# Kernel optimization log

Hardware: AMD Instinct MI355X
Metric: run time of the kernel (lower is better)

Reference implementation:

```python
import jax, jax.numpy as jnp
import numpy as np
from math import sqrt, pi

EMBED, HEADS, ATTN, MLP = 1024, 16, 1024, 4096
HEAD_DIM = ATTN // HEADS
EPS = 1e-5

def _ln(x):
    mu = jnp.mean(x, axis=-1, keepdims=True)
    var = jnp.var(x, axis=-1, keepdims=True)
    return (x - mu) / jnp.sqrt(var + EPS)

def _gelu(x):
    return 0.5 * x * (1.0 + jnp.tanh(sqrt(2.0 / pi) * (x + 0.044715 * x**3)))

def setup_inputs() -> dict:
    key = jax.random.key(0)
    ks = jax.random.split(key, 6)
    B, S = 2, 2048
    x = jax.random.normal(ks[0], (B, S, EMBED), dtype=jnp.float32)
    # weights stored as [in, out] (transpose of torch's [out, in]); math identical
    w_qkv = jax.random.normal(ks[1], (EMBED, 3 * ATTN), dtype=jnp.float32) / sqrt(EMBED)
    w_fc = jax.random.normal(ks[2], (ATTN, EMBED), dtype=jnp.float32) / sqrt(ATTN)
    w1 = jax.random.normal(ks[3], (EMBED, MLP), dtype=jnp.float32) / sqrt(EMBED)
    b1 = jnp.zeros((MLP,), dtype=jnp.float32)
    w2 = jax.random.normal(ks[4], (MLP, EMBED), dtype=jnp.float32) / sqrt(MLP)
    b2 = jnp.zeros((EMBED,), dtype=jnp.float32)
    return {"x": x, "w_qkv": w_qkv, "w_fc": w_fc, "w1": w1, "b1": b1, "w2": w2, "b2": b2}

def reference(x, w_qkv, w_fc, w1, b1, w2, b2):
    B, S, _ = x.shape
    res = x
    h = _ln(x)
    qkv = h @ w_qkv                                   # [B,S,3*ATTN]
    q, k, v = jnp.split(qkv, 3, axis=-1)
    q = q.reshape(B, S, HEADS, HEAD_DIM)
    k = k.reshape(B, S, HEADS, HEAD_DIM)
    v = v.reshape(B, S, HEADS, HEAD_DIM)
    attn = jnp.einsum('bqnc,bknc->bnqk', q, k) / sqrt(HEAD_DIM)  # [B,H,S,S]
    attn = jax.nn.softmax(attn, axis=-1)
    attn_val = jnp.einsum('bnqk,bknc->bqnc', attn, v).reshape(B, S, ATTN)
    x = res + attn_val @ w_fc
    res = x
    h = _ln(x)
    h = _gelu(h @ w1 + b1) @ w2 + b2
    return res + h
```

## Files before the change

kernel.cpp:

```cpp
#include <hip/hip_runtime.h>

typedef unsigned short u16;
typedef __attribute__((ext_vector_type(8))) short bf16x8;
typedef __attribute__((ext_vector_type(4))) short s16x4;
typedef __attribute__((ext_vector_type(4))) float f32x4;

#define DEV __device__ __forceinline__

DEV u16 f2bf(float f) {
  union { float f; unsigned u; } v; v.f = f;
  unsigned r = v.u + 0x7fffu + ((v.u >> 16) & 1u);
  return (u16)(r >> 16);
}
DEV u16 f2bf_tr(float f) {
  union { float f; unsigned u; } v; v.f = f;
  return (u16)(v.u >> 16);
}

DEV int swzi(int row, int col) { return row * 64 + (col ^ ((row & 7) << 3)); }

DEV void gl16(const u16* g, u16* l) {
  __builtin_amdgcn_global_load_lds((const __attribute__((address_space(1))) void*)g,
                                   (__attribute__((address_space(3))) void*)l, 16, 0, 0);
}

template <int N> DEV void waitv() {
  asm volatile("s_waitcnt vmcnt(%0)" :: "n"(N) : "memory");
}

__global__ __launch_bounds__(256) void wcastT(const float* __restrict__ w,
                                              u16* __restrict__ wt, int K, int N) {
  __shared__ float t[32][33];
  int n0 = blockIdx.x * 32, k0 = blockIdx.y * 32;
  int tx = threadIdx.x & 31, ty = threadIdx.x >> 5;
#pragma unroll
  for (int i = 0; i < 32; i += 8)
    t[ty + i][tx] = w[(size_t)(k0 + ty + i) * N + n0 + tx];
  __syncthreads();
#pragma unroll
  for (int i = 0; i < 32; i += 8)
    wt[(size_t)(n0 + ty + i) * K + k0 + tx] = f2bf(t[tx][ty + i]);
}

__global__ __launch_bounds__(256) void ln_kernel(const float* __restrict__ x,
                                                 u16* __restrict__ out) {
  int row = blockIdx.x, tid = threadIdx.x;
  const float4* xr = (const float4*)(x + (size_t)row * 1024);
  float4 f = xr[tid];
  float s = f.x + f.y + f.z + f.w;
  float s2 = f.x * f.x + f.y * f.y + f.z * f.z + f.w * f.w;
#pragma unroll
  for (int o = 1; o < 64; o <<= 1) { s += __shfl_xor(s, o); s2 += __shfl_xor(s2, o); }
  __shared__ float red[2][4];
  int wid = tid >> 6;
  if ((tid & 63) == 0) { red[0][wid] = s; red[1][wid] = s2; }
  __syncthreads();
  float tot  = red[0][0] + red[0][1] + red[0][2] + red[0][3];
  float tot2 = red[1][0] + red[1][1] + red[1][2] + red[1][3];
  float mu = tot * (1.0f / 1024.0f);
  float var = tot2 * (1.0f / 1024.0f) - mu * mu;
  float rstd = rsqrtf(var + 1e-5f);
  s16x4 o4;
  o4[0] = (short)f2bf((f.x - mu) * rstd);
  o4[1] = (short)f2bf((f.y - mu) * rstd);
  o4[2] = (short)f2bf((f.z - mu) * rstd);
  o4[3] = (short)f2bf((f.w - mu) * rstd);
  *(s16x4*)(out + (size_t)row * 1024 + tid * 4) = o4;
}

template <int MODE, int BM, int BK>
__global__ __launch_bounds__(256) void gemm_bt(
    const u16* __restrict__ A, const u16* __restrict__ Bt, int N, int K,
    const float* __restrict__ resid, const float* __restrict__ bias,
    float* __restrict__ outF, u16* __restrict__ o0, u16* __restrict__ o1,
    u16* __restrict__ o2) {
  constexpr int MR = BM / 32;
  constexpr int KH = BK / 32;
  constexpr int LDEPTH = KH * (BM / 64 + 2);
  constexpr int ACH = BM * 32, BCH = 128 * 32;
  __shared__ __align__(16) u16 lA[2 * KH * ACH];
  __shared__ __align__(16) u16 lB[2 * KH * BCH];
  int tid = threadIdx.x;
  int lane = tid & 63, wid = tid >> 6;
  int lr = lane & 15, lg = lane >> 4;

  int gx = gridDim.x;
  int nwg = gx * gridDim.y;
  int bid = blockIdx.y * gx + blockIdx.x;
  int swz = (bid & 7) * (nwg >> 3) + (bid >> 3);
  int rowBase = (swz / gx) * BM, colBase = (swz % gx) * 128;
  int wr = (wid >> 1) * (MR * 16), wc = (wid & 1) * 64;

  int srow = wid * 16 + (lane >> 2);
  int scol = (lane & 3) * 8;
  const u16* gA = A + (size_t)(rowBase + srow) * K + scol;
  const u16* gB = Bt + (size_t)(colBase + srow) * K + scol;
  u16* lAb = &lA[wid * 16 * 32];
  u16* lBb = &lB[wid * 16 * 32];

  auto stage = [&](int t, int buf) {
    int k0 = t * BK;
#pragma unroll
    for (int kk = 0; kk < KH; kk++) {
      u16* dA = lAb + buf * KH * ACH + kk * ACH;
      u16* dB = lBb + buf * KH * BCH + kk * BCH;
      int koff = k0 + kk * 32;
#pragma unroll
      for (int c = 0; c < BM / 64; c++)
        gl16(gA + (size_t)c * 64 * K + koff, dA + c * 64 * 32);
#pragma unroll
      for (int c = 0; c < 2; c++)
        gl16(gB + (size_t)c * 64 * K + koff, dB + c * 64 * 32);
    }
  };

  f32x4 acc[MR][4];
  f32x4 zero = {0.f, 0.f, 0.f, 0.f};
#pragma unroll
  for (int m = 0; m < MR; m++)
#pragma unroll
    for (int n = 0; n < 4; n++) acc[m][n] = zero;

  stage(0, 0);

  int nt = K / BK;
  for (int t = 0; t < nt; t++) {
    int cur = t & 1;
    if (t + 1 < nt) {
      stage(t + 1, cur ^ 1);
      waitv<LDEPTH>();
    } else {
      waitv<0>();
    }
    __builtin_amdgcn_s_barrier();
    asm volatile("" ::: "memory");

    const u16* cA = &lA[cur * KH * ACH];
    const u16* cB = &lB[cur * KH * BCH];
#pragma unroll
    for (int kk = 0; kk < KH; kk++) {
      bf16x8 af[MR], bfv[4];
#pragma unroll
      for (int m = 0; m < MR; m++)
        af[m] = *(const bf16x8*)&cA[kk * ACH + (wr + m * 16 + lr) * 32 + lg * 8];
#pragma unroll
      for (int n = 0; n < 4; n++)
        bfv[n] = *(const bf16x8*)&cB[kk * BCH + (wc + n * 16 + lr) * 32 + lg * 8];
#pragma unroll
      for (int m = 0; m < MR; m++)
#pragma unroll
        for (int n = 0; n < 4; n++)
          acc[m][n] = __builtin_amdgcn_mfma_f32_16x16x32_bf16(bfv[n], af[m], acc[m][n], 0, 0, 0);
    }

    asm volatile("" ::: "memory");
    __builtin_amdgcn_s_barrier();
  }

#pragma unroll
  for (int m = 0; m < MR; m++) {
    int grow = rowBase + wr + m * 16 + lr;
#pragma unroll
    for (int n = 0; n < 4; n++) {
      int gcol = colBase + wc + n * 16 + lg * 4;
      f32x4 v4 = acc[m][n];
      if constexpr (MODE == 0) {
        if (gcol < 2048) {
          bool isq = gcol < 1024;
          u16* dst = isq ? o0 : o1;
          s16x4 o4;
#pragma unroll
          for (int j = 0; j < 4; j++)
            o4[j] = (short)f2bf(isq ? v4[j] * 0.18033688011112042f : v4[j]);
          *(s16x4*)&dst[(size_t)grow * 1024 + (gcol & 1023)] = o4;
        } else {
          int c = gcol - 2048;
          int bb = grow >> 11, ss = grow & 2047;
          size_t vbase = ((size_t)bb * 1024 + c) * 2048 + ss;
#pragma unroll
          for (int j = 0; j < 4; j++)
            o2[vbase + (size_t)j * 2048] = f2bf(v4[j]);
        }
      } else if constexpr (MODE == 1) {
        size_t idx = (size_t)grow * N + gcol;
        float4 r = *(const float4*)&resid[idx];
        float4 ov = {r.x + v4[0], r.y + v4[1], r.z + v4[2], r.w + v4[3]};
        *(float4*)&outF[idx] = ov;
      } else if constexpr (MODE == 2) {
        float4 bq = *(const float4*)&bias[gcol];
        s16x4 o4;
#pragma unroll
        for (int j = 0; j < 4; j++) {
          float g = v4[j] + ((const float*)&bq)[j];
          float e = __builtin_amdgcn_exp2f(2.302208198f * (g + 0.044715f * g * g * g));
          o4[j] = (short)f2bf(g - g * __builtin_amdgcn_rcpf(1.0f + e));
        }
        *(s16x4*)&o0[(size_t)grow * N + gcol] = o4;
      } else {
        size_t idx = (size_t)grow * N + gcol;
        float4 r = *(const float4*)&resid[idx];
        float4 bq = *(const float4*)&bias[gcol];
        float4 ov = {r.x + bq.x + v4[0], r.y + bq.y + v4[1],
                     r.z + bq.z + v4[2], r.w + bq.w + v4[3]};
        *(float4*)&outF[idx] = ov;
      }
    }
  }
}

__global__ __launch_bounds__(256) void attn_kernel(const u16* __restrict__ q,
                                                   const u16* __restrict__ k,
                                                   const u16* __restrict__ vt,
                                                   u16* __restrict__ o) {
  __shared__ __align__(16) u16 lK[64 * 64];
  __shared__ __align__(16) u16 lV[64 * 64];
  __shared__ __align__(16) u16 lP[4 * 2 * 16 * 64];
  const int S = 2048, E = 1024;
  int qt = blockIdx.x, h = blockIdx.y, b = blockIdx.z;
  int tid = threadIdx.x, wid = tid >> 6, lane = tid & 63;
  int lr = lane & 15, lg = lane >> 4;
  u16* lPw = &lP[wid * 2048];

  const u16* qp = q + ((size_t)b * S + qt * 128 + wid * 32) * E + h * 64;
  const u16* kp = k + (size_t)b * S * E + h * 64;
  const u16* vp = vt + ((size_t)(b * 16 + h) * 64) * S;

  bf16x8 aQ[2][2];
#pragma unroll
  for (int m = 0; m < 2; m++)
#pragma unroll
    for (int kk = 0; kk < 2; kk++)
      aQ[m][kk] = *(const bf16x8*)(qp + (size_t)(m * 16 + lr) * E + kk * 32 + lg * 8);

  bf16x8 onesv;
#pragma unroll
  for (int i = 0; i < 8; i++) onesv[i] = (short)0x3F80;

  f32x4 accO[2][4], accL[2];
  f32x4 zero = {0.f, 0.f, 0.f, 0.f};
#pragma unroll
  for (int m = 0; m < 2; m++) {
    accL[m] = zero;
#pragma unroll
    for (int nn = 0; nn < 4; nn++) accO[m][nn] = zero;
  }

  int sr_ = tid >> 3, sc_ = (tid & 7) * 8;
  const u16* kps0 = kp + (size_t)sr_ * E + sc_;
  const u16* kps1 = kp + (size_t)(sr_ + 32) * E + sc_;
  const u16* vps0 = vp + (size_t)sr_ * S + sc_;
  const u16* vps1 = vp + (size_t)(sr_ + 32) * S + sc_;

  bf16x8 rk0 = *(const bf16x8*)(kps0);
  bf16x8 rk1 = *(const bf16x8*)(kps1);
  bf16x8 rv0 = *(const bf16x8*)(vps0);
  bf16x8 rv1 = *(const bf16x8*)(vps1);

  for (int kv0 = 0; kv0 < S; kv0 += 64) {
    __syncthreads();
    *(bf16x8*)&lK[swzi(sr_, sc_)] = rk0;
    *(bf16x8*)&lK[swzi(32 + sr_, sc_)] = rk1;
    *(bf16x8*)&lV[swzi(sr_, sc_)] = rv0;
    *(bf16x8*)&lV[swzi(32 + sr_, sc_)] = rv1;
    int nx = kv0 + 64;
    if (nx < S) {
      rk0 = *(const bf16x8*)(kps0 + (size_t)nx * E);
      rk1 = *(const bf16x8*)(kps1 + (size_t)nx * E);
      rv0 = *(const bf16x8*)(vps0 + nx);
      rv1 = *(const bf16x8*)(vps1 + nx);
    }
    __syncthreads();

    f32x4 sc4[2][4];
#pragma unroll
    for (int m = 0; m < 2; m++)
#pragma unroll
      for (int n = 0; n < 4; n++) sc4[m][n] = zero;
#pragma unroll
    for (int n = 0; n < 4; n++) {
      bf16x8 bk0 = *(const bf16x8*)&lK[swzi(n * 16 + lr, lg * 8)];
      bf16x8 bk1 = *(const bf16x8*)&lK[swzi(n * 16 + lr, 32 + lg * 8)];
#pragma unroll
      for (int m = 0; m < 2; m++) {
        sc4[m][n] = __builtin_amdgcn_mfma_f32_16x16x32_bf16(bk0, aQ[m][0], sc4[m][n], 0, 0, 0);
        sc4[m][n] = __builtin_amdgcn_mfma_f32_16x16x32_bf16(bk1, aQ[m][1], sc4[m][n], 0, 0, 0);
      }
    }

#pragma unroll
    for (int m = 0; m < 2; m++)
#pragma unroll
      for (int n = 0; n < 4; n++) {
        s16x4 pq;
#pragma unroll
        for (int j = 0; j < 4; j++)
          pq[j] = (short)f2bf_tr(__builtin_amdgcn_exp2f(sc4[m][n][j]));
        *(s16x4*)&lPw[m * 1024 + swzi(lr, n * 16 + lg * 4)] = pq;
      }

#pragma unroll
    for (int kk = 0; kk < 2; kk++) {
      bf16x8 ap[2];
#pragma unroll
      for (int m = 0; m < 2; m++)
        ap[m] = *(const bf16x8*)&lPw[m * 1024 + swzi(lr, kk * 32 + lg * 8)];
#pragma unroll
      for (int m = 0; m < 2; m++)
        accL[m] = __builtin_amdgcn_mfma_f32_16x16x32_bf16(onesv, ap[m], accL[m], 0, 0, 0);
#pragma unroll
      for (int nn = 0; nn < 4; nn++) {
        bf16x8 bv = *(const bf16x8*)&lV[swzi(nn * 16 + lr, kk * 32 + lg * 8)];
#pragma unroll
        for (int m = 0; m < 2; m++)
          accO[m][nn] = __builtin_amdgcn_mfma_f32_16x16x32_bf16(bv, ap[m], accO[m][nn], 0, 0, 0);
      }
    }
  }

#pragma unroll
  for (int m = 0; m < 2; m++) {
    float inv = 1.0f / accL[m][0];
    int srow = qt * 128 + wid * 32 + m * 16 + lr;
#pragma unroll
    for (int nn = 0; nn < 4; nn++) {
      s16x4 o4;
#pragma unroll
      for (int j = 0; j < 4; j++) o4[j] = (short)f2bf(accO[m][nn][j] * inv);
      *(s16x4*)&o[((size_t)b * S + srow) * E + h * 64 + nn * 16 + lg * 4] = o4;
    }
  }
}

extern "C" void kernel_launch(void* const* d_in, const int* in_sizes, int n_in,
                              void* d_out, int out_size, void* d_ws, size_t ws_size,
                              hipStream_t stream) {
  (void)in_sizes; (void)n_in; (void)out_size; (void)ws_size;
  const float* x     = (const float*)d_in[0];
  const float* w_qkv = (const float*)d_in[1];
  const float* w_fc  = (const float*)d_in[2];
  const float* w1    = (const float*)d_in[3];
  const float* b1    = (const float*)d_in[4];
  const float* w2    = (const float*)d_in[5];
  const float* b2    = (const float*)d_in[6];
  float* out = (float*)d_out;
  char* ws = (char*)d_ws;

  u16* wqkvT = (u16*)(ws);
  u16* wfcT  = (u16*)(ws + 6291456);
  u16* w1T   = (u16*)(ws + 8388608);
  u16* w2T   = (u16*)(ws + 16777216);
  u16* hbuf  = (u16*)(ws + 25165824);
  u16* qbuf  = (u16*)(ws + 33554432);
  u16* kbuf  = (u16*)(ws + 41943040);
  u16* vtbuf = (u16*)(ws + 58720256);
  float* x2  = (float*)(ws + 67108864);
  u16* act   = qbuf;

  wcastT<<<dim3(96, 32), 256, 0, stream>>>(w_qkv, wqkvT, 1024, 3072);
  wcastT<<<dim3(32, 32), 256, 0, stream>>>(w_fc, wfcT, 1024, 1024);
  wcastT<<<dim3(128, 32), 256, 0, stream>>>(w1, w1T, 1024, 4096);
  wcastT<<<dim3(32, 128), 256, 0, stream>>>(w2, w2T, 4096, 1024);

  ln_kernel<<<4096, 256, 0, stream>>>(x, hbuf);
  gemm_bt<0, 128, 32><<<dim3(24, 32), 256, 0, stream>>>(hbuf, wqkvT, 3072, 1024,
                                                        nullptr, nullptr, nullptr,
                                                        qbuf, kbuf, vtbuf);
  attn_kernel<<<dim3(16, 16, 2), 256, 0, stream>>>(qbuf, kbuf, vtbuf, hbuf);
  gemm_bt<1, 64, 64><<<dim3(8, 64), 256, 0, stream>>>(hbuf, wfcT, 1024, 1024,
                                                      x, nullptr, x2,
                                                      nullptr, nullptr, nullptr);
  ln_kernel<<<4096, 256, 0, stream>>>(x2, hbuf);
  gemm_bt<2, 128, 32><<<dim3(32, 32), 256, 0, stream>>>(hbuf, w1T, 4096, 1024,
                                                        nullptr, b1, nullptr,
                                                        act, nullptr, nullptr);
  gemm_bt<3, 64, 64><<<dim3(8, 64), 256, 0, stream>>>(act, w2T, 1024, 4096,
                                                      x2, b2, out,
                                                      nullptr, nullptr, nullptr);
}
```

Measured before the change: 244.2 us.

## Replace FFN up-projection GEMM with 256x256-tile, 8-wave pipelined kernel

Adds a dedicated 512-thread GEMM for the w1 projection with fused bias+GELU. Each block computes a 256x256 output tile and double-buffers LDS. Staging of the next K step is interleaved with four MFMA sub-phases, and s_setprio raises priority around the MFMA bursts. A grid swizzle is applied to block order. The aim is more operand reuse per LDS load and global loads hidden behind compute, in exchange for one block per CU (256 blocks), heavy register use and many barriers.

```diff
diff --git a/kernel.cpp b/kernel.cpp
--- a/kernel.cpp
+++ b/kernel.cpp
@@ -27,6 +27,11 @@
 template <int N> DEV void waitv() {
   asm volatile("s_waitcnt vmcnt(%0)" :: "n"(N) : "memory");
 }
+DEV void barrier_f() {
+  __builtin_amdgcn_s_barrier();
+  asm volatile("" ::: "memory");
+}
+DEV void lgkm0() { asm volatile("s_waitcnt lgkmcnt(0)" ::: "memory"); }
 
 __global__ __launch_bounds__(256) void wcastT(const float* __restrict__ w,
                                               u16* __restrict__ wt, int K, int N) {
@@ -132,8 +137,7 @@
     } else {
       waitv<0>();
     }
-    __builtin_amdgcn_s_barrier();
-    asm volatile("" ::: "memory");
+    barrier_f();
 
     const u16* cA = &lA[cur * KH * ACH];
     const u16* cB = &lB[cur * KH * BCH];
@@ -152,9 +156,7 @@
         for (int n = 0; n < 4; n++)
           acc[m][n] = __builtin_amdgcn_mfma_f32_16x16x32_bf16(bfv[n], af[m], acc[m][n], 0, 0, 0);
     }
-
-    asm volatile("" ::: "memory");
-    __builtin_amdgcn_s_barrier();
+    barrier_f();
   }
 
 #pragma unroll
@@ -186,16 +188,6 @@
         float4 r = *(const float4*)&resid[idx];
         float4 ov = {r.x + v4[0], r.y + v4[1], r.z + v4[2], r.w + v4[3]};
         *(float4*)&outF[idx] = ov;
-      } else if constexpr (MODE == 2) {
-        float4 bq = *(const float4*)&bias[gcol];
-        s16x4 o4;
-#pragma unroll
-        for (int j = 0; j < 4; j++) {
-          float g = v4[j] + ((const float*)&bq)[j];
-          float e = __builtin_amdgcn_exp2f(2.302208198f * (g + 0.044715f * g * g * g));
-          o4[j] = (short)f2bf(g - g * __builtin_amdgcn_rcpf(1.0f + e));
-        }
-        *(s16x4*)&o0[(size_t)grow * N + gcol] = o4;
       } else {
         size_t idx = (size_t)grow * N + gcol;
         float4 r = *(const float4*)&resid[idx];
@@ -204,6 +196,150 @@
                      r.z + bq.z + v4[2], r.w + bq.w + v4[3]};
         *(float4*)&outF[idx] = ov;
       }
+    }
+  }
+}
+
+__global__ __launch_bounds__(512, 1) void gemm256p(
+    const u16* __restrict__ A, const u16* __restrict__ Bt,
+    const float* __restrict__ bias, u16* __restrict__ o0) {
+  constexpr int K = 1024, N = 4096, NT = 16;
+  __shared__ __align__(16) u16 lA[2 * 2 * 256 * 32];
+  __shared__ __align__(16) u16 lB[2 * 2 * 256 * 32];
+  int tid = threadIdx.x;
+  int lane = tid & 63, wid = tid >> 6;
+  int lr = lane & 15, lg = lane >> 4;
+  int wm = wid >> 2, wn = wid & 3;
+
+  int gx = gridDim.x;
+  int nwg = gx * gridDim.y;
+  int bid = blockIdx.y * gx + blockIdx.x;
+  int swz = (bid & 7) * (nwg >> 3) + (bid >> 3);
+  int rowBase = (swz / gx) * 256, colBase = (swz % gx) * 256;
+
+  int sr0 = tid >> 2, sc = (tid & 3) * 8;
+  const u16* gA = A + (size_t)(rowBase + sr0) * K + sc;
+  const u16* gB = Bt + (size_t)(colBase + sr0) * K + sc;
+  u16* lAw = lA + wid * 512;
+  u16* lBw = lB + wid * 512;
+
+  auto stageA = [&](int t, int kh) {
+    int koff = t * 64 + kh * 32;
+    u16* d = lAw + ((t & 1) * 2 + kh) * 8192;
+    gl16(gA + koff, d);
+    gl16(gA + (size_t)128 * K + koff, d + 4096);
+  };
+  auto stageB = [&](int t, int kh) {
+    int koff = t * 64 + kh * 32;
+    u16* d = lBw + ((t & 1) * 2 + kh) * 8192;
+    gl16(gB + koff, d);
+    gl16(gB + (size_t)128 * K + koff, d + 4096);
+  };
+
+  f32x4 acc[8][4];
+  f32x4 zero = {0.f, 0.f, 0.f, 0.f};
+#pragma unroll
+  for (int m = 0; m < 8; m++)
+#pragma unroll
+    for (int n = 0; n < 4; n++) acc[m][n] = zero;
+
+  bf16x8 aF[4][2], bF0[2][2], bF1[2][2];
+
+  auto rdA = [&](int t, int rh) {
+#pragma unroll
+    for (int kh = 0; kh < 2; kh++) {
+      const u16* p = lA + ((t & 1) * 2 + kh) * 8192;
+#pragma unroll
+      for (int m = 0; m < 4; m++)
+        aF[m][kh] = *(const bf16x8*)&p[(wm * 128 + rh * 64 + m * 16 + lr) * 32 + lg * 8];
+    }
+  };
+  auto rdB = [&](bf16x8 (&bb)[2][2], int t, int ch) {
+#pragma unroll
+    for (int kh = 0; kh < 2; kh++) {
+      const u16* p = lB + ((t & 1) * 2 + kh) * 8192;
+#pragma unroll
+      for (int n = 0; n < 2; n++)
+        bb[n][kh] = *(const bf16x8*)&p[(wn * 64 + ch * 32 + n * 16 + lr) * 32 + lg * 8];
+    }
+  };
+
+  stageA(0, 0); stageA(0, 1); stageB(0, 0); stageB(0, 1);
+  waitv<2>();
+  barrier_f();
+
+  for (int t = 0; t < NT; t++) {
+    bool st = (t + 1 < NT);
+    rdA(t, 0); rdB(bF0, t, 0);
+    if (st) { stageA(t + 1, 0); stageA(t + 1, 1); }
+    barrier_f(); lgkm0();
+    __builtin_amdgcn_s_setprio(1);
+#pragma unroll
+    for (int m = 0; m < 4; m++)
+#pragma unroll
+      for (int n = 0; n < 2; n++)
+#pragma unroll
+        for (int kh = 0; kh < 2; kh++)
+          acc[m][n] = __builtin_amdgcn_mfma_f32_16x16x32_bf16(bF0[n][kh], aF[m][kh], acc[m][n], 0, 0, 0);
+    __builtin_amdgcn_s_setprio(0);
+    if (st) waitv<4>(); else waitv<0>();
+    barrier_f();
+    rdB(bF1, t, 1);
+    if (st) stageB(t + 1, 0);
+    barrier_f(); lgkm0();
+    __builtin_amdgcn_s_setprio(1);
+#pragma unroll
+    for (int m = 0; m < 4; m++)
+#pragma unroll
+      for (int n = 0; n < 2; n++)
+#pragma unroll
+        for (int kh = 0; kh < 2; kh++)
+          acc[m][2 + n] = __builtin_amdgcn_mfma_f32_16x16x32_bf16(bF1[n][kh], aF[m][kh], acc[m][2 + n], 0, 0, 0);
+    __builtin_amdgcn_s_setprio(0);
+    barrier_f();
+    rdA(t, 1);
+    if (st) stageB(t + 1, 1);
+    barrier_f(); lgkm0();
+    __builtin_amdgcn_s_setprio(1);
+#pragma unroll
+    for (int m = 0; m < 4; m++)
+#pragma unroll
+      for (int n = 0; n < 2; n++)
+#pragma unroll
+        for (int kh = 0; kh < 2; kh++)
+          acc[4 + m][n] = __builtin_amdgcn_mfma_f32_16x16x32_bf16(bF0[n][kh], aF[m][kh], acc[4 + m][n], 0, 0, 0);
+    __builtin_amdgcn_s_setprio(0);
+    barrier_f();
+    barrier_f(); lgkm0();
+    __builtin_amdgcn_s_setprio(1);
+#pragma unroll
+    for (int m = 0; m < 4; m++)
+#pragma unroll
+      for (int n = 0; n < 2; n++)
+#pragma unroll
+        for (int kh = 0; kh < 2; kh++)
+          acc[4 + m][2 + n] = __builtin_amdgcn_mfma_f32_16x16x32_bf16(bF1[n][kh], aF[m][kh], acc[4 + m][2 + n], 0, 0, 0);
+    __builtin_amdgcn_s_setprio(0);
+    if (st) waitv<2>();
+    barrier_f();
+  }
+
+#pragma unroll
+  for (int mi = 0; mi < 8; mi++) {
+    int grow = rowBase + wm * 128 + mi * 16 + lr;
+#pragma unroll
+    for (int ni = 0; ni < 4; ni++) {
+      int gcol = colBase + wn * 64 + ni * 16 + lg * 4;
+      f32x4 v4 = acc[mi][ni];
+      float4 bq = *(const float4*)&bias[gcol];
+      s16x4 o4;
+#pragma unroll
+      for (int j = 0; j < 4; j++) {
+        float g = v4[j] + ((const float*)&bq)[j];
+        float e = __builtin_amdgcn_exp2f(2.302208198f * (g + 0.044715f * g * g * g));
+        o4[j] = (short)f2bf(g - g * __builtin_amdgcn_rcpf(1.0f + e));
+      }
+      *(s16x4*)&o0[(size_t)grow * N + gcol] = o4;
     }
   }
 }
@@ -370,9 +506,7 @@
                                                       x, nullptr, x2,
                                                       nullptr, nullptr, nullptr);
   ln_kernel<<<4096, 256, 0, stream>>>(x2, hbuf);
-  gemm_bt<2, 128, 32><<<dim3(32, 32), 256, 0, stream>>>(hbuf, w1T, 4096, 1024,
-                                                        nullptr, b1, nullptr,
-                                                        act, nullptr, nullptr);
+  gemm256p<<<dim3(16, 16), 512, 0, stream>>>(hbuf, w1T, b1, act);
   gemm_bt<3, 64, 64><<<dim3(8, 64), 256, 0, stream>>>(act, w2T, 1024, 4096,
                                                       x2, b2, out,
                                                       nullptr, nullptr, nullptr);
```

Result: faster. 235.7 us (median of 2 runs) (-3.5%).
